# Optimization experiments

Measured on AMD Instinct MI355X. Metric: run time of the kernel, lower is better.

Reference implementation:

```python
import jax, jax.numpy as jnp
import numpy as np

K = 256
HEADS = 4

def setup_inputs() -> dict:
    key = jax.random.key(0)
    ks = jax.random.split(key, 6)
    x = jax.random.normal(ks[0], (4, 4096, K), dtype=jnp.float32)
    scale = 1.0 / np.sqrt(K)
    Wq = jax.random.normal(ks[1], (K, K), dtype=jnp.float32) * scale
    Wk = jax.random.normal(ks[2], (K, K), dtype=jnp.float32) * scale
    Wv = jax.random.normal(ks[3], (K, K), dtype=jnp.float32) * scale
    Wu = jax.random.normal(ks[4], (K, K), dtype=jnp.float32) * scale
    bu = jax.random.normal(ks[5], (K,), dtype=jnp.float32) * scale
    return {"x": x, "Wq": Wq, "Wk": Wk, "Wv": Wv, "Wu": Wu, "bu": bu}

def reference(x, Wq, Wk, Wv, Wu, bu):
    b, t, e = x.shape
    h = HEADS
    s = e // h
    # torch Linear: y = x @ W.T
    q = (x @ Wq.T).reshape(b, t, h, s)
    k = (x @ Wk.T).reshape(b, t, h, s)
    v = (x @ Wv.T).reshape(b, t, h, s)
    # scores: [b, h, t, t]
    dot = jnp.einsum('bihs,bjhs->bhij', q, k) / jnp.sqrt(jnp.float32(s))
    # NOTE: original code calls masked_fill (non in-place) and discards the
    # result, so the causal mask has NO effect. Faithful: no mask.
    attn = jax.nn.softmax(dot, axis=-1)
    out = jnp.einsum('bhij,bjhs->bihs', attn, v).reshape(b, t, e)
    return out @ Wu.T + bu
```

## Files before the change

### kernel.cpp

```cpp
#include <hip/hip_runtime.h>

typedef unsigned short u16;
typedef __attribute__((ext_vector_type(8))) __bf16 bf16x8;
typedef __attribute__((ext_vector_type(4))) float f32x4;
typedef __attribute__((ext_vector_type(4))) unsigned int u32x4;
typedef __attribute__((ext_vector_type(2))) unsigned int u32x2;

#define GLD16(g, l) __builtin_amdgcn_global_load_lds( \
    (const __attribute__((address_space(1))) unsigned int*)(g), \
    (__attribute__((address_space(3))) unsigned int*)(l), 16, 0, 0)

__device__ __forceinline__ u16 f2bf(float f) {
    unsigned u = __builtin_bit_cast(unsigned, f);
    unsigned r = u + 0x7fffu + ((u >> 16) & 1u);
    return (u16)(r >> 16);
}

__global__ __launch_bounds__(256) void cvt_bf16(const float* __restrict__ src,
                                                u16* __restrict__ dst, int n8) {
    int i = blockIdx.x * 256 + threadIdx.x;
    if (i >= n8) return;
    const float4* s = (const float4*)src;
    float4 a = s[2 * i], b = s[2 * i + 1];
    union { u16 u[8]; u32x4 v; } o;
    o.u[0] = f2bf(a.x); o.u[1] = f2bf(a.y); o.u[2] = f2bf(a.z); o.u[3] = f2bf(a.w);
    o.u[4] = f2bf(b.x); o.u[5] = f2bf(b.y); o.u[6] = f2bf(b.z); o.u[7] = f2bf(b.w);
    ((u32x4*)dst)[i] = o.v;
}

__global__ __launch_bounds__(256) void cvt_w4(const float* __restrict__ Wq,
                                              const float* __restrict__ Wk,
                                              const float* __restrict__ Wv,
                                              const float* __restrict__ Wu,
                                              u16* __restrict__ dst, float qscale) {
    int i = blockIdx.x * 256 + threadIdx.x;
    int widx = i >> 13, j = i & 8191;
    const float* src = (widx == 0) ? Wq : (widx == 1) ? Wk : (widx == 2) ? Wv : Wu;
    float scale = (widx == 0) ? qscale : 1.0f;
    const float4* s = (const float4*)src;
    float4 a = s[2 * j], b = s[2 * j + 1];
    union { u16 u[8]; u32x4 v; } o;
    o.u[0] = f2bf(a.x * scale); o.u[1] = f2bf(a.y * scale);
    o.u[2] = f2bf(a.z * scale); o.u[3] = f2bf(a.w * scale);
    o.u[4] = f2bf(b.x * scale); o.u[5] = f2bf(b.y * scale);
    o.u[6] = f2bf(b.z * scale); o.u[7] = f2bf(b.w * scale);
    ((u32x4*)dst)[i] = o.v;
}

template <int F32OUT>
__device__ __forceinline__ void gemm_core(const u16* __restrict__ A,
                                          const u16* __restrict__ B,
                                          void* __restrict__ Cout,
                                          const float* __restrict__ bias,
                                          size_t ldc, int mblk, int nblk,
                                          u16* As, u16* Bs) {
    const int tid = threadIdx.x;
    const int w = tid >> 6, l = tid & 63;
    const int lo = l & 15, hi = l >> 4;
    const size_t m0 = (size_t)mblk * 128;
    const int n0 = nblk * 128;
    const int wm = (w >> 1) * 64, wn = (w & 1) * 64;

    f32x4 acc[4][4] = {};

    {
#pragma unroll
        for (int i = 0; i < 2; ++i) {
            int cidx = (w * 2 + i) * 64 + l;
            int row = cidx >> 2, c = cidx & 3;
            GLD16(A + (m0 + row) * 256 + c * 8, &As[(w * 2 + i) * 512]);
            GLD16(B + (size_t)(n0 + row) * 256 + c * 8, &Bs[(w * 2 + i) * 512]);
        }
    }
    int buf = 0;
#pragma unroll 1
    for (int k0 = 0; k0 < 8; ++k0) {
        __syncthreads();
        if (k0 < 7) {
#pragma unroll
            for (int i = 0; i < 2; ++i) {
                int cidx = (w * 2 + i) * 64 + l;
                int row = cidx >> 2, c = cidx & 3;
                GLD16(A + (m0 + row) * 256 + (k0 + 1) * 32 + c * 8, &As[(buf ^ 1) * 4096 + (w * 2 + i) * 512]);
                GLD16(B + (size_t)(n0 + row) * 256 + (k0 + 1) * 32 + c * 8, &Bs[(buf ^ 1) * 4096 + (w * 2 + i) * 512]);
            }
        }
        bf16x8 af[4], bg[4];
#pragma unroll
        for (int mt = 0; mt < 4; ++mt)
            af[mt] = *(const bf16x8*)&As[buf * 4096 + (wm + mt * 16 + lo) * 32 + hi * 8];
#pragma unroll
        for (int nt = 0; nt < 4; ++nt)
            bg[nt] = *(const bf16x8*)&Bs[buf * 4096 + (wn + nt * 16 + lo) * 32 + hi * 8];
        __builtin_amdgcn_s_setprio(1);
#pragma unroll
        for (int mt = 0; mt < 4; ++mt)
#pragma unroll
            for (int nt = 0; nt < 4; ++nt)
                acc[mt][nt] = __builtin_amdgcn_mfma_f32_16x16x32_bf16(af[mt], bg[nt], acc[mt][nt], 0, 0, 0);
        __builtin_amdgcn_s_setprio(0);
        buf ^= 1;
    }

    const int r0 = hi * 4;
#pragma unroll
    for (int mt = 0; mt < 4; ++mt) {
#pragma unroll
        for (int nt = 0; nt < 4; ++nt) {
            int col = n0 + wn + nt * 16 + lo;
#pragma unroll
            for (int r = 0; r < 4; ++r) {
                size_t row = m0 + wm + mt * 16 + r0 + r;
                if (F32OUT) {
                    ((float*)Cout)[row * ldc + col] = acc[mt][nt][r] + bias[col];
                } else {
                    ((u16*)Cout)[row * ldc + col] = f2bf(acc[mt][nt][r]);
                }
            }
        }
    }
}

__global__ __launch_bounds__(256) void gemm_qkv(const u16* __restrict__ xb,
                                                const u16* __restrict__ wqb,
                                                const u16* __restrict__ wkb,
                                                const u16* __restrict__ wvb,
                                                u16* __restrict__ qb,
                                                u16* __restrict__ kb,
                                                u16* __restrict__ vtb) {
    __shared__ u16 As[2 * 4096];
    __shared__ u16 Bs[2 * 4096];
    if (blockIdx.z == 0)
        gemm_core<0>(xb, wqb, qb, nullptr, 256, blockIdx.x, blockIdx.y, As, Bs);
    else if (blockIdx.z == 1)
        gemm_core<0>(xb, wkb, kb, nullptr, 256, blockIdx.x, blockIdx.y, As, Bs);
    else
        gemm_core<0>(wvb, xb, vtb, nullptr, 16384, blockIdx.y, blockIdx.x, As, Bs);
}

template <int F32OUT>
__global__ __launch_bounds__(256) void gemm_one(const u16* __restrict__ A,
                                                const u16* __restrict__ B,
                                                void* __restrict__ C,
                                                const float* __restrict__ bias,
                                                size_t ldc) {
    __shared__ u16 As[2 * 4096];
    __shared__ u16 Bs[2 * 4096];
    gemm_core<F32OUT>(A, B, C, bias, ldc, blockIdx.x, blockIdx.y, As, Bs);
}

__global__ __launch_bounds__(256, 2) void attn_fwd(const u16* __restrict__ qb,
                                                   const u16* __restrict__ kb,
                                                   const u16* __restrict__ vtb,
                                                   u16* __restrict__ attb) {
    __shared__ u16 Ks[3][64 * 64];
    __shared__ u16 Vs[3][64 * 64];
    __shared__ u16 Ps[4][32 * 64];
    const int tid = threadIdx.x, w = tid >> 6, l = tid & 63;
    const int lo = l & 15, hi = l >> 4;

    int lin = blockIdx.y * gridDim.x + blockIdx.x;
    int nid = (lin & 7) * 64 + (lin >> 3);
    const int bh = nid >> 5, qblk = nid & 31;
    const int b = bh >> 2, h = bh & 3;
    const int qbase = qblk * 128 + w * 32;

    bf16x8 qf[2][2];
#pragma unroll
    for (int mt = 0; mt < 2; ++mt)
#pragma unroll
        for (int ks = 0; ks < 2; ++ks)
            qf[mt][ks] = *(const bf16x8*)&qb[(size_t)(b * 4096 + qbase + mt * 16 + lo) * 256 + h * 64 + ks * 32 + hi * 8];

    bf16x8 ones;
#pragma unroll
    for (int j = 0; j < 8; ++j) ones[j] = (__bf16)1.0f;

    f32x4 o[2][4] = {};
    f32x4 osum[2] = {};
    const f32x4 fz = {0.f, 0.f, 0.f, 0.f};

    auto stage = [&](int sb, int kt) {
#pragma unroll
        for (int i = 0; i < 2; ++i) {
            int cidx = (w * 2 + i) * 64 + l;
            int row = cidx >> 3, c = cidx & 7;
            int sc = c ^ (row & 7);
            GLD16(kb + (size_t)(b * 4096 + kt * 64 + row) * 256 + h * 64 + sc * 8,
                  &Ks[sb][(w * 2 + i) * 512]);
            GLD16(vtb + (size_t)(h * 64 + row) * 16384 + (size_t)b * 4096 + kt * 64 + sc * 8,
                  &Vs[sb][(w * 2 + i) * 512]);
        }
    };

    stage(0, 0);
    stage(1, 1);
#pragma unroll 1
    for (int kt = 0; kt < 64; ++kt) {
        if (kt < 63) { asm volatile("s_waitcnt vmcnt(4)" ::: "memory"); }
        else         { asm volatile("s_waitcnt vmcnt(0)" ::: "memory"); }
        __builtin_amdgcn_s_barrier();
        if (kt < 62) stage((kt + 2) % 3, kt + 2);
        const int sl = kt % 3;

        f32x4 s[2][4];
        {
            bf16x8 kf[4];
#pragma unroll
            for (int nt = 0; nt < 4; ++nt) {
                int key = nt * 16 + lo;
                int pc = hi ^ (key & 7);
                kf[nt] = *(const bf16x8*)&Ks[sl][key * 64 + pc * 8];
            }
            __builtin_amdgcn_s_setprio(1);
#pragma unroll
            for (int mt = 0; mt < 2; ++mt)
#pragma unroll
                for (int nt = 0; nt < 4; ++nt)
                    s[mt][nt] = __builtin_amdgcn_mfma_f32_16x16x32_bf16(kf[nt], qf[mt][0], fz, 0, 0, 0);
            __builtin_amdgcn_s_setprio(0);
        }
        {
            bf16x8 kf[4];
#pragma unroll
            for (int nt = 0; nt < 4; ++nt) {
                int key = nt * 16 + lo;
                int pc = (4 + hi) ^ (key & 7);
                kf[nt] = *(const bf16x8*)&Ks[sl][key * 64 + pc * 8];
            }
            __builtin_amdgcn_s_setprio(1);
#pragma unroll
            for (int mt = 0; mt < 2; ++mt)
#pragma unroll
                for (int nt = 0; nt < 4; ++nt)
                    s[mt][nt] = __builtin_amdgcn_mfma_f32_16x16x32_bf16(kf[nt], qf[mt][1], s[mt][nt], 0, 0, 0);
            __builtin_amdgcn_s_setprio(0);
        }

#pragma unroll
        for (int mt = 0; mt < 2; ++mt) {
#pragma unroll
            for (int nt = 0; nt < 4; ++nt) {
                union { __bf16 bb[4]; u32x2 v; } pw;
#pragma unroll
                for (int r = 0; r < 4; ++r)
                    pw.bb[r] = (__bf16)__builtin_amdgcn_exp2f(s[mt][nt][r]);
                *(u32x2*)&Ps[w][(mt * 16 + lo) * 64 + (((nt * 4 + hi) ^ lo) << 2)] = pw.v;
            }
        }
        asm volatile("s_waitcnt lgkmcnt(0)" ::: "memory");

#pragma unroll
        for (int ks2 = 0; ks2 < 2; ++ks2) {
            bf16x8 vf[4];
#pragma unroll
            for (int dt = 0; dt < 4; ++dt) {
                int dr = dt * 16 + lo;
                vf[dt] = *(const bf16x8*)&Vs[sl][dr * 64 + (((ks2 * 4 + hi) ^ (dr & 7)) << 3)];
            }
            union { u32x2 c[2]; bf16x8 v; } pA, pB;
            pA.c[0] = *(const u32x2*)&Ps[w][(0 + lo) * 64 + (((ks2 * 8 + hi * 2 + 0) ^ lo) << 2)];
            pA.c[1] = *(const u32x2*)&Ps[w][(0 + lo) * 64 + (((ks2 * 8 + hi * 2 + 1) ^ lo) << 2)];
            pB.c[0] = *(const u32x2*)&Ps[w][(16 + lo) * 64 + (((ks2 * 8 + hi * 2 + 0) ^ lo) << 2)];
            pB.c[1] = *(const u32x2*)&Ps[w][(16 + lo) * 64 + (((ks2 * 8 + hi * 2 + 1) ^ lo) << 2)];
            __builtin_amdgcn_s_setprio(1);
#pragma unroll
            for (int dt = 0; dt < 4; ++dt)
                o[0][dt] = __builtin_amdgcn_mfma_f32_16x16x32_bf16(vf[dt], pA.v, o[0][dt], 0, 0, 0);
#pragma unroll
            for (int dt = 0; dt < 4; ++dt)
                o[1][dt] = __builtin_amdgcn_mfma_f32_16x16x32_bf16(vf[dt], pB.v, o[1][dt], 0, 0, 0);
            osum[0] = __builtin_amdgcn_mfma_f32_16x16x32_bf16(ones, pA.v, osum[0], 0, 0, 0);
            osum[1] = __builtin_amdgcn_mfma_f32_16x16x32_bf16(ones, pB.v, osum[1], 0, 0, 0);
            __builtin_amdgcn_s_setprio(0);
        }
    }

#pragma unroll
    for (int mt = 0; mt < 2; ++mt) {
        float inv = __builtin_amdgcn_rcpf(osum[mt][0]);
        size_t row = (size_t)(b * 4096 + qbase + mt * 16 + lo);
#pragma unroll
        for (int dt = 0; dt < 4; ++dt) {
            union { __bf16 bb[4]; u32x2 v; } ob;
#pragma unroll
            for (int r = 0; r < 4; ++r) ob.bb[r] = (__bf16)(o[mt][dt][r] * inv);
            *(u32x2*)&attb[row * 256 + h * 64 + dt * 16 + hi * 4] = ob.v;
        }
    }
}

extern "C" void kernel_launch(void* const* d_in, const int* in_sizes, int n_in,
                              void* d_out, int out_size, void* d_ws, size_t ws_size,
                              hipStream_t stream) {
    const float* x  = (const float*)d_in[0];
    const float* Wq = (const float*)d_in[1];
    const float* Wk = (const float*)d_in[2];
    const float* Wv = (const float*)d_in[3];
    const float* Wu = (const float*)d_in[4];
    const float* bu = (const float*)d_in[5];

    char* ws = (char*)d_ws;
    u16* xb  = (u16*)ws;
    u16* qb  = (u16*)(ws + (8u << 20));
    u16* kb  = (u16*)(ws + (16u << 20));
    u16* vtb = (u16*)(ws + (24u << 20));
    u16* wqb = (u16*)(ws + (32u << 20));
    u16* wkb = wqb + 65536;
    u16* wvb = wkb + 65536;
    u16* wub = wvb + 65536;
    u16* attb = xb;

    const float kLog2eOver8 = 0.18033688011112042f;

    cvt_bf16<<<2048, 256, 0, stream>>>(x, xb, in_sizes[0] / 8);
    cvt_w4<<<128, 256, 0, stream>>>(Wq, Wk, Wv, Wu, wqb, kLog2eOver8);

    gemm_qkv<<<dim3(128, 2, 3), 256, 0, stream>>>(xb, wqb, wkb, wvb, qb, kb, vtb);

    attn_fwd<<<dim3(32, 16), 256, 0, stream>>>(qb, kb, vtb, attb);

    gemm_one<1><<<dim3(128, 2), 256, 0, stream>>>(attb, wub, d_out, bu, 256);
}
```

Measured before the change: 126.2 us.

## Load K/V fragments directly into registers with double-buffered prefetch, dropping LDS staging

Removes the shared-memory K and V tiles and the async global-to-LDS staging with barriers. Each wave now loads its own K and V MFMA fragments straight from global memory into registers, ping-ponging two register buffers so the next tile's load overlaps the current tile's compute. This removes block-wide barriers and LDS traffic. In exchange, each of the four waves re-reads the same K/V tiles from global/L2, which quadruples that traffic, and the extra buffers raise VGPR pressure under a two-blocks-per-CU launch bound.

```diff
diff --git a/kernel.cpp b/kernel.cpp
--- a/kernel.cpp
+++ b/kernel.cpp
@@ -153,8 +153,6 @@
                                                    const u16* __restrict__ kb,
                                                    const u16* __restrict__ vtb,
                                                    u16* __restrict__ attb) {
-    __shared__ u16 Ks[3][64 * 64];
-    __shared__ u16 Vs[3][64 * 64];
     __shared__ u16 Ps[4][32 * 64];
     const int tid = threadIdx.x, w = tid >> 6, l = tid & 63;
     const int lo = l & 15, hi = l >> 4;
@@ -180,62 +178,38 @@
     f32x4 osum[2] = {};
     const f32x4 fz = {0.f, 0.f, 0.f, 0.f};
 
-    auto stage = [&](int sb, int kt) {
-#pragma unroll
-        for (int i = 0; i < 2; ++i) {
-            int cidx = (w * 2 + i) * 64 + l;
-            int row = cidx >> 3, c = cidx & 7;
-            int sc = c ^ (row & 7);
-            GLD16(kb + (size_t)(b * 4096 + kt * 64 + row) * 256 + h * 64 + sc * 8,
-                  &Ks[sb][(w * 2 + i) * 512]);
-            GLD16(vtb + (size_t)(h * 64 + row) * 16384 + (size_t)b * 4096 + kt * 64 + sc * 8,
-                  &Vs[sb][(w * 2 + i) * 512]);
-        }
+    const u16* kbase = kb + (size_t)(b * 4096 + lo) * 256 + h * 64 + hi * 8;
+    const u16* vbase = vtb + (size_t)(h * 64 + lo) * 16384 + (size_t)b * 4096 + hi * 8;
+
+    auto loadKV = [&](int kt, bf16x8 (&kr)[2][4], bf16x8 (&vr)[2][4]) {
+        const u16* kp = kbase + (size_t)kt * 64 * 256;
+        const u16* vp = vbase + kt * 64;
+#pragma unroll
+        for (int ks = 0; ks < 2; ++ks)
+#pragma unroll
+            for (int nt = 0; nt < 4; ++nt)
+                kr[ks][nt] = *(const bf16x8*)(kp + (size_t)nt * 16 * 256 + ks * 32);
+#pragma unroll
+        for (int ks2 = 0; ks2 < 2; ++ks2)
+#pragma unroll
+            for (int dt = 0; dt < 4; ++dt)
+                vr[ks2][dt] = *(const bf16x8*)(vp + (size_t)dt * 16 * 16384 + ks2 * 32);
     };
 
-    stage(0, 0);
-    stage(1, 1);
-#pragma unroll 1
-    for (int kt = 0; kt < 64; ++kt) {
-        if (kt < 63) { asm volatile("s_waitcnt vmcnt(4)" ::: "memory"); }
-        else         { asm volatile("s_waitcnt vmcnt(0)" ::: "memory"); }
-        __builtin_amdgcn_s_barrier();
-        if (kt < 62) stage((kt + 2) % 3, kt + 2);
-        const int sl = kt % 3;
-
+    auto compute = [&](const bf16x8 (&kr)[2][4], const bf16x8 (&vr)[2][4]) {
         f32x4 s[2][4];
-        {
-            bf16x8 kf[4];
-#pragma unroll
-            for (int nt = 0; nt < 4; ++nt) {
-                int key = nt * 16 + lo;
-                int pc = hi ^ (key & 7);
-                kf[nt] = *(const bf16x8*)&Ks[sl][key * 64 + pc * 8];
-            }
-            __builtin_amdgcn_s_setprio(1);
-#pragma unroll
-            for (int mt = 0; mt < 2; ++mt)
-#pragma unroll
-                for (int nt = 0; nt < 4; ++nt)
-                    s[mt][nt] = __builtin_amdgcn_mfma_f32_16x16x32_bf16(kf[nt], qf[mt][0], fz, 0, 0, 0);
-            __builtin_amdgcn_s_setprio(0);
-        }
-        {
-            bf16x8 kf[4];
-#pragma unroll
-            for (int nt = 0; nt < 4; ++nt) {
-                int key = nt * 16 + lo;
-                int pc = (4 + hi) ^ (key & 7);
-                kf[nt] = *(const bf16x8*)&Ks[sl][key * 64 + pc * 8];
-            }
-            __builtin_amdgcn_s_setprio(1);
-#pragma unroll
-            for (int mt = 0; mt < 2; ++mt)
-#pragma unroll
-                for (int nt = 0; nt < 4; ++nt)
-                    s[mt][nt] = __builtin_amdgcn_mfma_f32_16x16x32_bf16(kf[nt], qf[mt][1], s[mt][nt], 0, 0, 0);
-            __builtin_amdgcn_s_setprio(0);
-        }
+        __builtin_amdgcn_s_setprio(1);
+#pragma unroll
+        for (int mt = 0; mt < 2; ++mt)
+#pragma unroll
+            for (int nt = 0; nt < 4; ++nt)
+                s[mt][nt] = __builtin_amdgcn_mfma_f32_16x16x32_bf16(kr[0][nt], qf[mt][0], fz, 0, 0, 0);
+#pragma unroll
+        for (int mt = 0; mt < 2; ++mt)
+#pragma unroll
+            for (int nt = 0; nt < 4; ++nt)
+                s[mt][nt] = __builtin_amdgcn_mfma_f32_16x16x32_bf16(kr[1][nt], qf[mt][1], s[mt][nt], 0, 0, 0);
+        __builtin_amdgcn_s_setprio(0);
 
 #pragma unroll
         for (int mt = 0; mt < 2; ++mt) {
@@ -252,12 +226,6 @@
 
 #pragma unroll
         for (int ks2 = 0; ks2 < 2; ++ks2) {
-            bf16x8 vf[4];
-#pragma unroll
-            for (int dt = 0; dt < 4; ++dt) {
-                int dr = dt * 16 + lo;
-                vf[dt] = *(const bf16x8*)&Vs[sl][dr * 64 + (((ks2 * 4 + hi) ^ (dr & 7)) << 3)];
-            }
             union { u32x2 c[2]; bf16x8 v; } pA, pB;
             pA.c[0] = *(const u32x2*)&Ps[w][(0 + lo) * 64 + (((ks2 * 8 + hi * 2 + 0) ^ lo) << 2)];
             pA.c[1] = *(const u32x2*)&Ps[w][(0 + lo) * 64 + (((ks2 * 8 + hi * 2 + 1) ^ lo) << 2)];
@@ -266,14 +234,24 @@
             __builtin_amdgcn_s_setprio(1);
 #pragma unroll
             for (int dt = 0; dt < 4; ++dt)
-                o[0][dt] = __builtin_amdgcn_mfma_f32_16x16x32_bf16(vf[dt], pA.v, o[0][dt], 0, 0, 0);
+                o[0][dt] = __builtin_amdgcn_mfma_f32_16x16x32_bf16(vr[ks2][dt], pA.v, o[0][dt], 0, 0, 0);
 #pragma unroll
             for (int dt = 0; dt < 4; ++dt)
-                o[1][dt] = __builtin_amdgcn_mfma_f32_16x16x32_bf16(vf[dt], pB.v, o[1][dt], 0, 0, 0);
+                o[1][dt] = __builtin_amdgcn_mfma_f32_16x16x32_bf16(vr[ks2][dt], pB.v, o[1][dt], 0, 0, 0);
             osum[0] = __builtin_amdgcn_mfma_f32_16x16x32_bf16(ones, pA.v, osum[0], 0, 0, 0);
             osum[1] = __builtin_amdgcn_mfma_f32_16x16x32_bf16(ones, pB.v, osum[1], 0, 0, 0);
             __builtin_amdgcn_s_setprio(0);
         }
+    };
+
+    bf16x8 kA[2][4], vA[2][4], kB[2][4], vB[2][4];
+    loadKV(0, kA, vA);
+#pragma unroll 1
+    for (int kt = 0; kt < 64; kt += 2) {
+        loadKV(kt + 1, kB, vB);
+        compute(kA, vA);
+        if (kt + 2 < 64) loadKV(kt + 2, kA, vA);
+        compute(kB, vB);
     }
 
 #pragma unroll
```

Measured after the change: 262.6 us. +108.1%, slower.
